# Kernel tuning notes

Hardware: AMD Instinct MI355X
Metric: run time of the kernel (lower is better)

## Reference

```python
import jax, jax.numpy as jnp
import numpy as np

# Coarse-to-fine lossless 3D segmentation (Seg3dLossless), batch=1, C=1.
RES = [17, 33, 65, 129]          # odd resolutions, stride (RF-1)/(R-1) is integral
RF = RES[-1]
B_MIN, B_MAX = -1.0, 1.0
BAL = 0.5                        # balance_value
N_CONFLICT_ITERS = 2             # fixed unroll of the data-dependent while-loop


def _mlp(pts, w1, b1, w2, b2, w3, b3):
    # query_func: occupancy MLP on normalized (x,y,z) points -> [N]
    h = jax.nn.relu(pts @ w1 + b1)
    h = jax.nn.relu(h @ w2 + b2)
    return jax.nn.sigmoid(h @ w3 + b3)[..., 0]


def _eval_grid(R, w1, b1, w2, b2, w3, b3):
    # batch_eval with align_corners=False: coords2D = (coord + 0.5)/RF, mapped to [B_MIN,B_MAX]
    s = (RF - 1) // (R - 1)
    c = jnp.arange(R, dtype=jnp.float32) * s                 # final-res integer coords
    p = (c + 0.5) / RF * (B_MAX - B_MIN) + B_MIN
    zz, yy, xx = jnp.meshgrid(p, p, p, indexing='ij')        # [D,H,W]
    pts = jnp.stack([xx, yy, zz], axis=-1).reshape(-1, 3)    # (x,y,z) order
    return _mlp(pts, w1, b1, w2, b2, w3, b3).reshape(R, R, R)


def _resize(x, R):
    # trilinear, align_corners=True: out index j -> in coord j*(in-1)/(out-1)
    c = jnp.linspace(0.0, x.shape[0] - 1.0, R)
    zz, yy, xx = jnp.meshgrid(c, c, c, indexing='ij')
    return jax.scipy.ndimage.map_coordinates(x, [zz, yy, xx], order=1, mode='nearest')


def _dilate(m):
    # smooth_conv3x3 (mean filter) followed by >0 == 3x3x3 binary dilation
    f = jax.lax.reduce_window(m.astype(jnp.float32), 0.0, jax.lax.max,
                              (3, 3, 3), (1, 1, 1), 'SAME')
    return f > 0.0


def setup_inputs() -> dict:
    key = jax.random.key(0)
    k1, k2, k3 = jax.random.split(key, 3)
    H = 64
    return {
        'w1': jax.random.normal(k1, (3, H), jnp.float32) * 0.8,
        'b1': jnp.zeros((H,), jnp.float32),
        'w2': jax.random.normal(k2, (H, H), jnp.float32) * (1.0 / np.sqrt(H)),
        'b2': jnp.zeros((H,), jnp.float32),
        'w3': jax.random.normal(k3, (H, 1), jnp.float32) * (1.0 / np.sqrt(H)),
        'b3': jnp.zeros((1,), jnp.float32),
    }


def reference(w1, b1, w2, b2, w3, b3):
    params = (w1, b1, w2, b2, w3, b3)
    # level 0: dense eval on the coarse grid
    occ = _eval_grid(RES[0], *params)                        # [R0,R0,R0]
    s0 = (RF - 1) // (RES[0] - 1)
    calculated = jnp.zeros((RF, RF, RF), bool).at[::s0, ::s0, ::s0].set(True)

    for R in RES[1:]:
        s = (RF - 1) // (R - 1)
        valid = _resize((occ > BAL).astype(jnp.float32), R)  # no-grad mask path
        occ_i = _resize(occ, R)                              # differentiable interp
        boundary = _dilate((valid > 0.0) & (valid < 1.0))
        calc_l = calculated[::s, ::s, ::s]
        boundary = boundary & (~calc_l)                      # skip already-evaluated voxels
        occ_true = _eval_grid(R, *params)                    # query_func at this level
        occ = jnp.where(boundary, occ_true, occ_i)           # scatter of occupancys_topk
        calc_l = calc_l | boundary
        # conflict resolution: re-query 3^3 neighbors of sign-flip voxels
        conflict = boundary & ((occ_i - BAL) * (occ_true - BAL) < 0.0)
        for _ in range(N_CONFLICT_ITERS):
            nbr = _dilate(conflict) & (~calc_l)
            occ_prev = occ
            occ = jnp.where(nbr, occ_true, occ)
            calc_l = calc_l | nbr
            conflict = nbr & ((occ_prev - BAL) * (occ_true - BAL) < 0.0)
        calculated = calculated.at[::s, ::s, ::s].set(calc_l)

    return occ[None, None]                                   # (1, 1, D, H, W)
```

## Files before the change

### kernel.cpp

```cpp
#include <hip/hip_runtime.h>

#define HH 64

static __global__ void k_set_ones(unsigned char* __restrict__ p, int n){
  int i = blockIdx.x * blockDim.x + threadIdx.x;
  if (i < n) p[i] = 1;
}

static __global__ void k_prep_w2t(const float* __restrict__ w2, float* __restrict__ w2t){
  int t = blockIdx.x * 256 + threadIdx.x;
  w2t[t] = w2[(t & 63) * HH + (t >> 6)];
}

__device__ __forceinline__ float mlp_eval(
    const float* __restrict__ w1, const float* __restrict__ b1,
    const float* __restrict__ w2t, const float* __restrict__ b2,
    const float* __restrict__ w3, const float* __restrict__ b3,
    float x, float y, float z)
{
  float h1[HH];
  #pragma unroll
  for (int i = 0; i < HH; ++i){
    float v = b1[i];
    v = fmaf(x, w1[i],        v);
    v = fmaf(y, w1[HH + i],   v);
    v = fmaf(z, w1[2*HH + i], v);
    h1[i] = fmaxf(v, 0.0f);
  }
  float o = b3[0];
  #pragma unroll 2
  for (int j = 0; j < HH; ++j){
    float acc = b2[j];
    const float* wr = &w2t[j*HH];
    #pragma unroll
    for (int k = 0; k < HH; ++k) acc = fmaf(h1[k], wr[k], acc);
    o = fmaf(fmaxf(acc, 0.0f), w3[j], o);
  }
  return 1.0f / (1.0f + expf(-o));
}

static __global__ __launch_bounds__(256, 4) void k_eval_mlp(
    const float* __restrict__ w1, const float* __restrict__ b1,
    const float* __restrict__ w2t, const float* __restrict__ b2,
    const float* __restrict__ w3, const float* __restrict__ b3,
    float* __restrict__ out, int R, int s)
{
  const unsigned int n = (unsigned int)R * (unsigned int)R * (unsigned int)R;
  unsigned int pid = blockIdx.x * 256u + threadIdx.x;
  if (pid >= n) return;
  const unsigned int c = pid % (unsigned int)R;
  const unsigned int r = pid / (unsigned int)R;
  const unsigned int b = r % (unsigned int)R;
  const unsigned int a = r / (unsigned int)R;
  const float inv129x2 = 2.0f / 129.0f;
  const float x = ((float)(c * (unsigned int)s) + 0.5f) * inv129x2 - 1.0f;
  const float y = ((float)(b * (unsigned int)s) + 0.5f) * inv129x2 - 1.0f;
  const float z = ((float)(a * (unsigned int)s) + 0.5f) * inv129x2 - 1.0f;
  out[pid] = mlp_eval(w1, b1, w2t, b2, w3, b3, x, y, z);
}

static __global__ __launch_bounds__(256, 4) void k_eval_sparse(
    const float* __restrict__ w1, const float* __restrict__ b1,
    const float* __restrict__ w2t, const float* __restrict__ b2,
    const float* __restrict__ w3, const float* __restrict__ b3,
    const int* __restrict__ idxl, const unsigned int* __restrict__ cnt,
    const float* __restrict__ occ_i,
    float* __restrict__ out, unsigned char* __restrict__ mism,
    int R, int s, unsigned int n)
{
  unsigned int count = *cnt;
  if (count > n) count = n;
  const unsigned int slot = blockIdx.x * 256u + threadIdx.x;
  if (slot >= count) return;
  const unsigned int pid = (unsigned int)idxl[slot];

  const unsigned int c = pid % (unsigned int)R;
  const unsigned int r = pid / (unsigned int)R;
  const unsigned int b = r % (unsigned int)R;
  const unsigned int a = r / (unsigned int)R;
  const float inv129x2 = 2.0f / 129.0f;
  const float x = ((float)(c * (unsigned int)s) + 0.5f) * inv129x2 - 1.0f;
  const float y = ((float)(b * (unsigned int)s) + 0.5f) * inv129x2 - 1.0f;
  const float z = ((float)(a * (unsigned int)s) + 0.5f) * inv129x2 - 1.0f;

  float ot = mlp_eval(w1, b1, w2t, b2, w3, b3, x, y, z);
  out[pid] = ot;
  mism[pid] = ((occ_i[pid] - 0.5f) * (ot - 0.5f) < 0.0f) ? (unsigned char)1 : (unsigned char)0;
}

static __global__ __launch_bounds__(256) void k_resize_b0(
    const float* __restrict__ prev,
    const unsigned char* __restrict__ calc_prev,
    float* __restrict__ occ_i,
    float* __restrict__ occ_out,
    unsigned char* __restrict__ bnd0,
    unsigned char* __restrict__ calc_out,
    unsigned char* __restrict__ confA,
    unsigned char* __restrict__ confB,
    unsigned char* __restrict__ upd,
    int R, int Rp)
{
  const unsigned int n = (unsigned int)R * (unsigned int)R * (unsigned int)R;
  unsigned int gid = blockIdx.x * 256u + threadIdx.x;
  if (gid >= n) return;
  int c = (int)(gid % (unsigned int)R);
  unsigned int r = gid / (unsigned int)R;
  int b = (int)(r % (unsigned int)R);
  int a = (int)(r / (unsigned int)R);
  int a0 = a >> 1, da = a & 1;
  int b0i = b >> 1, db = b & 1;
  int c0 = c >> 1, dc = c & 1;
  float sum = 0.0f;
  int cnt = 0;
  const int tot = (da + 1) * (db + 1) * (dc + 1);
  for (int dz = 0; dz <= da; ++dz)
    for (int dy = 0; dy <= db; ++dy)
      for (int dx = 0; dx <= dc; ++dx){
        float v = prev[((unsigned int)(a0 + dz) * (unsigned int)Rp + (unsigned int)(b0i + dy)) * (unsigned int)Rp + (unsigned int)(c0 + dx)];
        sum += v;
        cnt += (v > 0.5f) ? 1 : 0;
      }
  float oi = sum / (float)tot;
  occ_i[gid] = oi;
  occ_out[gid] = oi;
  bnd0[gid] = (cnt > 0 && cnt < tot) ? 1 : 0;
  calc_out[gid] = ((da | db | dc) == 0)
      ? calc_prev[((unsigned int)a0 * (unsigned int)Rp + (unsigned int)b0i) * (unsigned int)Rp + (unsigned int)c0]
      : (unsigned char)0;
  confA[gid] = 0; confB[gid] = 0; upd[gid] = 0;
}

static __global__ __launch_bounds__(256) void k_resize_boundary(
    const float* __restrict__ prev, const float* __restrict__ occ_true,
    const unsigned char* __restrict__ calc_prev,
    float* __restrict__ occ_i, float* __restrict__ occ_out,
    unsigned char* __restrict__ bnd0,
    unsigned char* __restrict__ mism, unsigned char* __restrict__ calc_out,
    int R, int Rp)
{
  const unsigned int n = (unsigned int)R * (unsigned int)R * (unsigned int)R;
  unsigned int gid = blockIdx.x * 256u + threadIdx.x;
  if (gid >= n) return;
  int c = (int)(gid % (unsigned int)R);
  unsigned int r = gid / (unsigned int)R;
  int b = (int)(r % (unsigned int)R);
  int a = (int)(r / (unsigned int)R);
  int a0 = a >> 1, da = a & 1;
  int b0i = b >> 1, db = b & 1;
  int c0 = c >> 1, dc = c & 1;
  float sum = 0.0f;
  int cnt = 0;
  const int tot = (da + 1) * (db + 1) * (dc + 1);
  for (int dz = 0; dz <= da; ++dz)
    for (int dy = 0; dy <= db; ++dy)
      for (int dx = 0; dx <= dc; ++dx){
        float v = prev[((unsigned int)(a0 + dz) * (unsigned int)Rp + (unsigned int)(b0i + dy)) * (unsigned int)Rp + (unsigned int)(c0 + dx)];
        sum += v;
        cnt += (v > 0.5f) ? 1 : 0;
      }
  float oi = sum / (float)tot;
  occ_i[gid] = oi;
  occ_out[gid] = oi;
  bnd0[gid] = (cnt > 0 && cnt < tot) ? 1 : 0;
  mism[gid] = ((oi - 0.5f) * (occ_true[gid] - 0.5f) < 0.0f) ? 1 : 0;
  calc_out[gid] = ((da | db | dc) == 0)
      ? calc_prev[((unsigned int)a0 * (unsigned int)Rp + (unsigned int)b0i) * (unsigned int)Rp + (unsigned int)c0]
      : (unsigned char)0;
}

static __global__ __launch_bounds__(256) void k_dil7x(
    const unsigned char* __restrict__ in, unsigned char* __restrict__ outp, int R)
{
  const unsigned int n = (unsigned int)R * (unsigned int)R * (unsigned int)R;
  unsigned int gid = blockIdx.x * 256u + threadIdx.x;
  if (gid >= n) return;
  int c = (int)(gid % (unsigned int)R);
  int g = (int)gid;
  int m = 0;
  #pragma unroll
  for (int d = -3; d <= 3; ++d){
    int q = c + d;
    if (q >= 0 && q < R) m |= in[g + d];
  }
  outp[gid] = (unsigned char)(m ? 1 : 0);
}

static __global__ __launch_bounds__(256) void k_dil7y(
    const unsigned char* __restrict__ in, unsigned char* __restrict__ outp, int R)
{
  const unsigned int n = (unsigned int)R * (unsigned int)R * (unsigned int)R;
  unsigned int gid = blockIdx.x * 256u + threadIdx.x;
  if (gid >= n) return;
  unsigned int r = gid / (unsigned int)R;
  int b = (int)(r % (unsigned int)R);
  int g = (int)gid;
  int m = 0;
  #pragma unroll
  for (int d = -3; d <= 3; ++d){
    int q = b + d;
    if (q >= 0 && q < R) m |= in[g + d * R];
  }
  outp[gid] = (unsigned char)(m ? 1 : 0);
}

static __global__ __launch_bounds__(256) void k_dil7z_count(
    const unsigned char* __restrict__ in, unsigned char* __restrict__ outp,
    unsigned int* __restrict__ bcnt, int R)
{
  const unsigned int n = (unsigned int)R * (unsigned int)R * (unsigned int)R;
  unsigned int gid = blockIdx.x * 256u + threadIdx.x;
  int m = 0;
  if (gid < n){
    int a = (int)(gid / ((unsigned int)R * (unsigned int)R));
    int g = (int)gid;
    int RR = R * R;
    #pragma unroll
    for (int d = -3; d <= 3; ++d){
      int q = a + d;
      if (q >= 0 && q < R) m |= in[g + d * RR];
    }
    outp[gid] = (unsigned char)(m ? 1 : 0);
  }
  unsigned long long bm = __ballot(m != 0);
  __shared__ unsigned int wc[4];
  int wid = (int)(threadIdx.x >> 6);
  if ((threadIdx.x & 63u) == 0) wc[wid] = (unsigned int)__popcll(bm);
  __syncthreads();
  if (threadIdx.x == 0) bcnt[blockIdx.x] = wc[0] + wc[1] + wc[2] + wc[3];
}

static __global__ __launch_bounds__(1024) void k_scan(
    unsigned int* __restrict__ bcnt, unsigned int nb, unsigned int* __restrict__ total)
{
  __shared__ unsigned int part[1024];
  const unsigned int t = threadIdx.x;
  const unsigned int chunk = (nb + 1023u) / 1024u;
  const unsigned int beg = t * chunk;
  const unsigned int end = (beg + chunk < nb) ? (beg + chunk) : nb;
  unsigned int s = 0;
  for (unsigned int i = beg; i < end; ++i) s += bcnt[i];
  part[t] = s;
  __syncthreads();
  for (int offd = 1; offd < 1024; offd <<= 1){
    unsigned int v = (t >= (unsigned int)offd) ? part[t - offd] : 0u;
    __syncthreads();
    part[t] += v;
    __syncthreads();
  }
  unsigned int run = (t == 0) ? 0u : part[t - 1];
  for (unsigned int i = beg; i < end; ++i){
    unsigned int v = bcnt[i];
    bcnt[i] = run;
    run += v;
  }
  if (t == 1023) *total = part[1023];
}

static __global__ __launch_bounds__(256) void k_scatter(
    const unsigned char* __restrict__ cand, const unsigned int* __restrict__ boff,
    int* __restrict__ idxl, unsigned int n)
{
  unsigned int gid = blockIdx.x * 256u + threadIdx.x;
  bool pred = (gid < n) && (cand[gid] != 0);
  unsigned long long m = __ballot(pred);
  __shared__ unsigned int wbase[4];
  int wid = (int)(threadIdx.x >> 6);
  int lane = (int)(threadIdx.x & 63u);
  if (lane == 0) wbase[wid] = (unsigned int)__popcll(m);
  __syncthreads();
  if (threadIdx.x == 0){
    unsigned int b = boff[blockIdx.x];
    unsigned int t0 = wbase[0], t1 = wbase[1], t2 = wbase[2];
    wbase[0] = b; wbase[1] = b + t0; wbase[2] = b + t0 + t1; wbase[3] = b + t0 + t1 + t2;
  }
  __syncthreads();
  if (pred){
    int pre = __popcll(m & ((1ull << lane) - 1ull));
    idxl[wbase[wid] + (unsigned int)pre] = (int)gid;
  }
}

static __global__ __launch_bounds__(256) void k_dilate_sparse(
    const int* __restrict__ idxl, const unsigned int* __restrict__ cnt,
    const unsigned char* __restrict__ src, const unsigned char* __restrict__ mism,
    unsigned char* __restrict__ calc, unsigned char* __restrict__ conf_out,
    unsigned char* __restrict__ upd, int R, int final_step,
    const float* __restrict__ occ_true, float* __restrict__ occ_out,
    unsigned int n)
{
  unsigned int count = *cnt;
  if (count > n) count = n;
  for (unsigned int slot = blockIdx.x * 256u + threadIdx.x; slot < count;
       slot += gridDim.x * 256u){
    int gid = idxl[slot];
    int c = gid % R;
    int r = gid / R;
    int b = r % R;
    int a = r / R;
    int m = 0;
    for (int dz = -1; dz <= 1; ++dz){
      int az = a + dz; if (az < 0 || az >= R) continue;
      for (int dy = -1; dy <= 1; ++dy){
        int by = b + dy; if (by < 0 || by >= R) continue;
        for (int dx = -1; dx <= 1; ++dx){
          int cx = c + dx; if (cx < 0 || cx >= R) continue;
          m |= src[(az * R + by) * R + cx];
        }
      }
    }
    unsigned char nb = (m && !calc[gid]) ? (unsigned char)1 : (unsigned char)0;
    conf_out[gid] = (nb && mism[gid]) ? (unsigned char)1 : (unsigned char)0;
    unsigned char u = upd[gid];
    if (nb){ calc[gid] = 1; if (!u){ upd[gid] = 1; u = 1; } }
    if (final_step && u) occ_out[gid] = occ_true[gid];
  }
}

static __global__ __launch_bounds__(256) void k_dilate_step(
    const unsigned char* __restrict__ src, const unsigned char* __restrict__ mism,
    unsigned char* __restrict__ calc, unsigned char* __restrict__ conf_out,
    unsigned char* __restrict__ upd, int R, int first, int final_step,
    const float* __restrict__ occ_true, float* __restrict__ occ_out)
{
  const unsigned int n = (unsigned int)R * (unsigned int)R * (unsigned int)R;
  unsigned int gid = blockIdx.x * 256u + threadIdx.x;
  if (gid >= n) return;
  int c = (int)(gid % (unsigned int)R);
  unsigned int r = gid / (unsigned int)R;
  int b = (int)(r % (unsigned int)R);
  int a = (int)(r / (unsigned int)R);
  int m = 0;
  for (int dz = -1; dz <= 1; ++dz){
    int az = a + dz; if (az < 0 || az >= R) continue;
    for (int dy = -1; dy <= 1; ++dy){
      int by = b + dy; if (by < 0 || by >= R) continue;
      for (int dx = -1; dx <= 1; ++dx){
        int cx = c + dx; if (cx < 0 || cx >= R) continue;
        m |= src[((unsigned int)az * (unsigned int)R + (unsigned int)by) * (unsigned int)R + (unsigned int)cx];
      }
    }
  }
  unsigned char nb = (m && !calc[gid]) ? (unsigned char)1 : (unsigned char)0;
  if (nb) calc[gid] = 1;
  conf_out[gid] = (nb && mism[gid]) ? (unsigned char)1 : (unsigned char)0;
  unsigned char u;
  if (first){ u = nb; upd[gid] = nb; }
  else { u = upd[gid]; if (nb && !u){ upd[gid] = 1; u = 1; } }
  if (final_step && u) occ_out[gid] = occ_true[gid];
}

extern "C" void kernel_launch(void* const* d_in, const int* in_sizes, int n_in,
                              void* d_out, int out_size, void* d_ws, size_t ws_size,
                              hipStream_t stream)
{
  const float* w1 = (const float*)d_in[0];
  const float* b1 = (const float*)d_in[1];
  const float* w2 = (const float*)d_in[2];
  const float* b2 = (const float*)d_in[3];
  const float* w3 = (const float*)d_in[4];
  const float* b3 = (const float*)d_in[5];
  float* out = (float*)d_out;

  const int NF = 129 * 129 * 129;
  const int NP = 65 * 65 * 65;
  char* ws = (char*)d_ws;
  size_t off = 0;
  auto alloc = [&](size_t bytes) -> void* {
    void* p = (void*)(ws + off);
    off += (bytes + 255) & ~(size_t)255;
    return p;
  };
  float* f_true  = (float*)alloc((size_t)NF * 4);
  float* f_occi  = (float*)alloc((size_t)NF * 4);
  float* f_prevA = (float*)alloc((size_t)NP * 4);
  float* f_prevB = (float*)alloc((size_t)NP * 4);
  float* f_w2t   = (float*)alloc((size_t)HH * HH * 4);
  int*   i_idx   = (int*)alloc((size_t)NF * 4);
  unsigned int* u_cnt  = (unsigned int*)alloc(256);
  unsigned int* u_bcnt = (unsigned int*)alloc(8448 * 4);
  unsigned char* b_b0    = (unsigned char*)alloc(NF);
  unsigned char* b_mism  = (unsigned char*)alloc(NF);
  unsigned char* b_confA = (unsigned char*)alloc(NF);
  unsigned char* b_confB = (unsigned char*)alloc(NF);
  unsigned char* b_calcA = (unsigned char*)alloc(NF);
  unsigned char* b_calcB = (unsigned char*)alloc(NF);
  unsigned char* b_upd   = (unsigned char*)alloc(NF);
  unsigned char* b_cand  = (unsigned char*)alloc(NF);
  unsigned char* b_tmp   = (unsigned char*)alloc(NF);
  (void)ws_size;

  k_prep_w2t<<<16, 256, 0, stream>>>(w2, f_w2t);

  {
    int R = 17, s = 8;
    int n = R * R * R;
    int blocks = (n + 255) / 256;
    k_eval_mlp<<<blocks, 256, 0, stream>>>(w1, b1, f_w2t, b2, w3, b3, f_prevA, R, s);
    k_set_ones<<<blocks, 256, 0, stream>>>(b_calcA, n);
  }

  int Rp = 17;
  float* prev = f_prevA;
  unsigned char* calcP = b_calcA;
  unsigned char* calcC = b_calcB;
  for (int li = 1; li <= 3; ++li){
    int R = 2 * Rp - 1;
    int s = 128 / (R - 1);
    unsigned int n = (unsigned int)R * (unsigned int)R * (unsigned int)R;
    int blocks = (int)((n + 255u) / 256u);
    float* occ_out = (li == 3) ? out : ((prev == f_prevA) ? f_prevB : f_prevA);

    if (R == 33){
      k_eval_mlp<<<blocks, 256, 0, stream>>>(w1, b1, f_w2t, b2, w3, b3, f_true, R, s);
      k_resize_boundary<<<blocks, 256, 0, stream>>>(prev, f_true, calcP, f_occi, occ_out, b_b0, b_mism, calcC, R, Rp);
      k_dilate_step<<<blocks, 256, 0, stream>>>(b_b0,    b_mism, calcC, b_confA, b_upd, R, 1, 0, f_true, occ_out);
      k_dilate_step<<<blocks, 256, 0, stream>>>(b_confA, b_mism, calcC, b_confB, b_upd, R, 0, 0, f_true, occ_out);
      k_dilate_step<<<blocks, 256, 0, stream>>>(b_confB, b_mism, calcC, b_confA, b_upd, R, 0, 1, f_true, occ_out);
    } else {
      k_resize_b0<<<blocks, 256, 0, stream>>>(prev, calcP, f_occi, occ_out, b_b0, calcC,
                                              b_confA, b_confB, b_upd, R, Rp);
      k_dil7x<<<blocks, 256, 0, stream>>>(b_b0,  b_tmp,  R);
      k_dil7y<<<blocks, 256, 0, stream>>>(b_tmp, b_cand, R);
      k_dil7z_count<<<blocks, 256, 0, stream>>>(b_cand, b_tmp, u_bcnt, R);
      k_scan<<<1, 1024, 0, stream>>>(u_bcnt, (unsigned int)blocks, u_cnt);
      k_scatter<<<blocks, 256, 0, stream>>>(b_tmp, u_bcnt, i_idx, n);
      k_eval_sparse<<<blocks, 256, 0, stream>>>(
          w1, b1, f_w2t, b2, w3, b3, i_idx, u_cnt, f_occi, f_true, b_mism, R, s, n);
      int sblocks = blocks < 4096 ? blocks : 4096;
      k_dilate_sparse<<<sblocks, 256, 0, stream>>>(i_idx, u_cnt, b_b0,    b_mism, calcC, b_confA, b_upd, R, 0, f_true, occ_out, n);
      k_dilate_sparse<<<sblocks, 256, 0, stream>>>(i_idx, u_cnt, b_confA, b_mism, calcC, b_confB, b_upd, R, 0, f_true, occ_out, n);
      k_dilate_sparse<<<sblocks, 256, 0, stream>>>(i_idx, u_cnt, b_confB, b_mism, calcC, b_confA, b_upd, R, 1, f_true, occ_out, n);
    }

    prev = occ_out;
    unsigned char* tmpc = calcP; calcP = calcC; calcC = tmpc;
    Rp = R;
  }
  (void)in_sizes; (void)n_in; (void)out_size;
}
```

Baseline: 353.6 us.

## Split MLP hidden dim across half-waves, stage weights in LDS, two points per thread

Restructures the MLP evaluation so each 64-lane wavefront processes 32 point pairs. Each half-wave computes half of the hidden-layer dot product from weights staged in shared memory, and the halves are combined with a cross-lane shuffle. Each thread evaluates two points, which halves the per-thread h1 register footprint and reuses every weight load across two points. The cost is redundant work in the upper half-lanes, a shuffle per output neuron, and shared-memory staging on every block, including sparse blocks that hold few valid points.

```diff
diff --git a/kernel.cpp b/kernel.cpp
--- a/kernel.cpp
+++ b/kernel.cpp
@@ -12,54 +12,117 @@
   w2t[t] = w2[(t & 63) * HH + (t >> 6)];
 }
 
-__device__ __forceinline__ float mlp_eval(
-    const float* __restrict__ w1, const float* __restrict__ b1,
-    const float* __restrict__ w2t, const float* __restrict__ b2,
-    const float* __restrict__ w3, const float* __restrict__ b3,
-    float x, float y, float z)
-{
-  float h1[HH];
+__device__ __forceinline__ void mlp_pair(
+    const float* __restrict__ sw1,
+    const float* __restrict__ sw2t,
+    const float* __restrict__ b2, const float* __restrict__ w3,
+    const float* __restrict__ b3,
+    float xA, float yA, float zA, float xB, float yB, float zB,
+    float& outA, float& outB)
+{
+  const int ibase = ((threadIdx.x & 63) >> 5) * 32;
+  float h1a[32], h1b[32];
   #pragma unroll
-  for (int i = 0; i < HH; ++i){
-    float v = b1[i];
-    v = fmaf(x, w1[i],        v);
-    v = fmaf(y, w1[HH + i],   v);
-    v = fmaf(z, w1[2*HH + i], v);
-    h1[i] = fmaxf(v, 0.0f);
-  }
-  float o = b3[0];
-  #pragma unroll 2
+  for (int k = 0; k < 32; k += 4){
+    const float4 wx = *(const float4*)&sw1[      ibase + k];
+    const float4 wy = *(const float4*)&sw1[ 64 + ibase + k];
+    const float4 wz = *(const float4*)&sw1[128 + ibase + k];
+    const float4 bb = *(const float4*)&sw1[192 + ibase + k];
+    h1a[k+0] = fmaxf(fmaf(xA,wx.x,fmaf(yA,wy.x,fmaf(zA,wz.x,bb.x))),0.f);
+    h1a[k+1] = fmaxf(fmaf(xA,wx.y,fmaf(yA,wy.y,fmaf(zA,wz.y,bb.y))),0.f);
+    h1a[k+2] = fmaxf(fmaf(xA,wx.z,fmaf(yA,wy.z,fmaf(zA,wz.z,bb.z))),0.f);
+    h1a[k+3] = fmaxf(fmaf(xA,wx.w,fmaf(yA,wy.w,fmaf(zA,wz.w,bb.w))),0.f);
+    h1b[k+0] = fmaxf(fmaf(xB,wx.x,fmaf(yB,wy.x,fmaf(zB,wz.x,bb.x))),0.f);
+    h1b[k+1] = fmaxf(fmaf(xB,wx.y,fmaf(yB,wy.y,fmaf(zB,wz.y,bb.y))),0.f);
+    h1b[k+2] = fmaxf(fmaf(xB,wx.z,fmaf(yB,wy.z,fmaf(zB,wz.z,bb.z))),0.f);
+    h1b[k+3] = fmaxf(fmaf(xB,wx.w,fmaf(yB,wy.w,fmaf(zB,wz.w,bb.w))),0.f);
+  }
+  float oa = b3[0], ob = oa;
+  #pragma unroll 1
   for (int j = 0; j < HH; ++j){
-    float acc = b2[j];
-    const float* wr = &w2t[j*HH];
+    const float4* wrow = (const float4*)&sw2t[j*HH + ibase];
+    float a0 = 0.f, a1 = 0.f, c0 = 0.f, c1 = 0.f;
     #pragma unroll
-    for (int k = 0; k < HH; ++k) acc = fmaf(h1[k], wr[k], acc);
-    o = fmaf(fmaxf(acc, 0.0f), w3[j], o);
-  }
-  return 1.0f / (1.0f + expf(-o));
-}
-
-static __global__ __launch_bounds__(256, 4) void k_eval_mlp(
+    for (int q = 0; q < 8; q += 2){
+      const float4 w0 = wrow[q];
+      const float4 w1q = wrow[q+1];
+      a0 = fmaf(h1a[4*q+0], w0.x, a0);
+      a0 = fmaf(h1a[4*q+1], w0.y, a0);
+      a0 = fmaf(h1a[4*q+2], w0.z, a0);
+      a0 = fmaf(h1a[4*q+3], w0.w, a0);
+      a1 = fmaf(h1a[4*q+4], w1q.x, a1);
+      a1 = fmaf(h1a[4*q+5], w1q.y, a1);
+      a1 = fmaf(h1a[4*q+6], w1q.z, a1);
+      a1 = fmaf(h1a[4*q+7], w1q.w, a1);
+      c0 = fmaf(h1b[4*q+0], w0.x, c0);
+      c0 = fmaf(h1b[4*q+1], w0.y, c0);
+      c0 = fmaf(h1b[4*q+2], w0.z, c0);
+      c0 = fmaf(h1b[4*q+3], w0.w, c0);
+      c1 = fmaf(h1b[4*q+4], w1q.x, c1);
+      c1 = fmaf(h1b[4*q+5], w1q.y, c1);
+      c1 = fmaf(h1b[4*q+6], w1q.z, c1);
+      c1 = fmaf(h1b[4*q+7], w1q.w, c1);
+    }
+    float accA = a0 + a1, accB = c0 + c1;
+    accA += __shfl_xor(accA, 32);
+    accB += __shfl_xor(accB, 32);
+    const float bj = b2[j], wj = w3[j];
+    oa = fmaf(fmaxf(accA + bj, 0.f), wj, oa);
+    ob = fmaf(fmaxf(accB + bj, 0.f), wj, ob);
+  }
+  outA = 1.f / (1.f + expf(-oa));
+  outB = 1.f / (1.f + expf(-ob));
+}
+
+#define STAGE_WEIGHTS()                                            \
+  __shared__ float sw1[4*HH];                                      \
+  __shared__ float sw2t[HH*HH];                                    \
+  {                                                                \
+    const int t0 = threadIdx.x;                                    \
+    if (t0 < 3*HH) sw1[t0] = w1[t0];                               \
+    else sw1[t0] = b1[t0 - 3*HH];                                  \
+    const float4* s4 = (const float4*)w2t;                         \
+    float4* d4 = (float4*)sw2t;                                    \
+    for (int i4 = t0; i4 < HH*HH/4; i4 += 256) d4[i4] = s4[i4];    \
+    __syncthreads();                                               \
+  }
+
+static __global__ __launch_bounds__(256)
+__attribute__((amdgpu_waves_per_eu(4,4)))
+void k_eval_mlp(
     const float* __restrict__ w1, const float* __restrict__ b1,
     const float* __restrict__ w2t, const float* __restrict__ b2,
     const float* __restrict__ w3, const float* __restrict__ b3,
     float* __restrict__ out, int R, int s)
 {
-  const unsigned int n = (unsigned int)R * (unsigned int)R * (unsigned int)R;
-  unsigned int pid = blockIdx.x * 256u + threadIdx.x;
-  if (pid >= n) return;
-  const unsigned int c = pid % (unsigned int)R;
-  const unsigned int r = pid / (unsigned int)R;
-  const unsigned int b = r % (unsigned int)R;
-  const unsigned int a = r / (unsigned int)R;
+  STAGE_WEIGHTS();
+  const unsigned int n = (unsigned int)R * (unsigned int)R * (unsigned int)R;
+  const int lane = threadIdx.x & 63;
+  const int wid = threadIdx.x >> 6;
+  const unsigned int base = blockIdx.x * 256u + (unsigned int)(wid * 64 + (lane & 31));
+  const unsigned int pidA = base < n ? base : (n - 1u);
+  const unsigned int pB = base + 32u;
+  const unsigned int pidB = pB < n ? pB : (n - 1u);
   const float inv129x2 = 2.0f / 129.0f;
-  const float x = ((float)(c * (unsigned int)s) + 0.5f) * inv129x2 - 1.0f;
-  const float y = ((float)(b * (unsigned int)s) + 0.5f) * inv129x2 - 1.0f;
-  const float z = ((float)(a * (unsigned int)s) + 0.5f) * inv129x2 - 1.0f;
-  out[pid] = mlp_eval(w1, b1, w2t, b2, w3, b3, x, y, z);
-}
-
-static __global__ __launch_bounds__(256, 4) void k_eval_sparse(
+  unsigned int cA = pidA % (unsigned int)R, rA = pidA / (unsigned int)R;
+  unsigned int cB = pidB % (unsigned int)R, rB = pidB / (unsigned int)R;
+  const float xA = ((float)(cA * (unsigned int)s) + 0.5f) * inv129x2 - 1.0f;
+  const float yA = ((float)((rA % (unsigned int)R) * (unsigned int)s) + 0.5f) * inv129x2 - 1.0f;
+  const float zA = ((float)((rA / (unsigned int)R) * (unsigned int)s) + 0.5f) * inv129x2 - 1.0f;
+  const float xB = ((float)(cB * (unsigned int)s) + 0.5f) * inv129x2 - 1.0f;
+  const float yB = ((float)((rB % (unsigned int)R) * (unsigned int)s) + 0.5f) * inv129x2 - 1.0f;
+  const float zB = ((float)((rB / (unsigned int)R) * (unsigned int)s) + 0.5f) * inv129x2 - 1.0f;
+  float oA, oB;
+  mlp_pair(sw1, sw2t, b2, w3, b3, xA, yA, zA, xB, yB, zB, oA, oB);
+  if ((threadIdx.x & 63) < 32){
+    if (base < n) out[pidA] = oA;
+    if (pB < n)   out[pidB] = oB;
+  }
+}
+
+static __global__ __launch_bounds__(256)
+__attribute__((amdgpu_waves_per_eu(4,4)))
+void k_eval_sparse(
     const float* __restrict__ w1, const float* __restrict__ b1,
     const float* __restrict__ w2t, const float* __restrict__ b2,
     const float* __restrict__ w3, const float* __restrict__ b3,
@@ -70,35 +133,45 @@
 {
   unsigned int count = *cnt;
   if (count > n) count = n;
-  const unsigned int slot = blockIdx.x * 256u + threadIdx.x;
-  if (slot >= count) return;
-  const unsigned int pid = (unsigned int)idxl[slot];
-
-  const unsigned int c = pid % (unsigned int)R;
-  const unsigned int r = pid / (unsigned int)R;
-  const unsigned int b = r % (unsigned int)R;
-  const unsigned int a = r / (unsigned int)R;
+  if (blockIdx.x * 256u >= count) return;
+  STAGE_WEIGHTS();
+  const int lane = threadIdx.x & 63;
+  const int wid = threadIdx.x >> 6;
+  const unsigned int slotA = blockIdx.x * 256u + (unsigned int)(wid * 64 + (lane & 31));
+  const unsigned int slotB = slotA + 32u;
+  const bool vA = slotA < count, vB = slotB < count;
+  const unsigned int pidA = (unsigned int)idxl[vA ? slotA : 0];
+  const unsigned int pidB = (unsigned int)idxl[vB ? slotB : 0];
   const float inv129x2 = 2.0f / 129.0f;
-  const float x = ((float)(c * (unsigned int)s) + 0.5f) * inv129x2 - 1.0f;
-  const float y = ((float)(b * (unsigned int)s) + 0.5f) * inv129x2 - 1.0f;
-  const float z = ((float)(a * (unsigned int)s) + 0.5f) * inv129x2 - 1.0f;
-
-  float ot = mlp_eval(w1, b1, w2t, b2, w3, b3, x, y, z);
-  out[pid] = ot;
-  mism[pid] = ((occ_i[pid] - 0.5f) * (ot - 0.5f) < 0.0f) ? (unsigned char)1 : (unsigned char)0;
+  unsigned int cA = pidA % (unsigned int)R, rA = pidA / (unsigned int)R;
+  unsigned int cB = pidB % (unsigned int)R, rB = pidB / (unsigned int)R;
+  const float xA = ((float)(cA * (unsigned int)s) + 0.5f) * inv129x2 - 1.0f;
+  const float yA = ((float)((rA % (unsigned int)R) * (unsigned int)s) + 0.5f) * inv129x2 - 1.0f;
+  const float zA = ((float)((rA / (unsigned int)R) * (unsigned int)s) + 0.5f) * inv129x2 - 1.0f;
+  const float xB = ((float)(cB * (unsigned int)s) + 0.5f) * inv129x2 - 1.0f;
+  const float yB = ((float)((rB % (unsigned int)R) * (unsigned int)s) + 0.5f) * inv129x2 - 1.0f;
+  const float zB = ((float)((rB / (unsigned int)R) * (unsigned int)s) + 0.5f) * inv129x2 - 1.0f;
+  float oA, oB;
+  mlp_pair(sw1, sw2t, b2, w3, b3, xA, yA, zA, xB, yB, zB, oA, oB);
+  if ((threadIdx.x & 63) < 32){
+    if (vA){
+      out[pidA] = oA;
+      mism[pidA] = ((occ_i[pidA] - 0.5f) * (oA - 0.5f) < 0.0f) ? (unsigned char)1 : (unsigned char)0;
+    }
+    if (vB){
+      out[pidB] = oB;
+      mism[pidB] = ((occ_i[pidB] - 0.5f) * (oB - 0.5f) < 0.0f) ? (unsigned char)1 : (unsigned char)0;
+    }
+  }
 }
 
 static __global__ __launch_bounds__(256) void k_resize_b0(
     const float* __restrict__ prev,
     const unsigned char* __restrict__ calc_prev,
-    float* __restrict__ occ_i,
-    float* __restrict__ occ_out,
-    unsigned char* __restrict__ bnd0,
-    unsigned char* __restrict__ calc_out,
-    unsigned char* __restrict__ confA,
-    unsigned char* __restrict__ confB,
-    unsigned char* __restrict__ upd,
-    int R, int Rp)
+    float* __restrict__ occ_i, float* __restrict__ occ_out,
+    unsigned char* __restrict__ bnd0, unsigned char* __restrict__ calc_out,
+    unsigned char* __restrict__ confA, unsigned char* __restrict__ confB,
+    unsigned char* __restrict__ upd, int R, int Rp)
 {
   const unsigned int n = (unsigned int)R * (unsigned int)R * (unsigned int)R;
   unsigned int gid = blockIdx.x * 256u + threadIdx.x;
```

Measured after the change: 308.0 us. 1.15x faster.
